# Kernel optimization log

Measured on AMD Instinct MI355X. Metric: run time of the kernel, lower is better.

The kernel has to match this reference:

```python
import jax, jax.numpy as jnp
import numpy as np

VOCAB_SIZE = 32000
PAD_IDX = 0


def setup_inputs() -> dict:
    key = jax.random.key(0)
    k1, k2 = jax.random.split(key)
    tokens = jax.random.randint(k1, (256, 2048), 0, VOCAB_SIZE, dtype=jnp.int64 if jax.config.jax_enable_x64 else jnp.int32)
    lengths = jax.random.randint(k2, (256,), 0, 2048, dtype=tokens.dtype)
    return {"tokens": tokens, "lengths": lengths}


def reference(tokens, lengths):
    # Faithful to torch OneHotEncoder.forward:
    #   onehot[b,t,:] = one_hot(tokens[b,t]) with pad_idx column zeroed per position,
    #   then summed over t -> counts [batch, vocab]. NOTE: the torch code computes a
    #   clamped `outhot` but RETURNS the un-clamped `onehot` counts; we match that.
    # Efficient form: direct per-row scatter-add histogram, skipping pad tokens,
    # without materializing the [B, T, V] intermediate.
    B, T = tokens.shape
    rows = jnp.arange(B)[:, None]  # [B,1] broadcasts against tokens [B,T]
    contrib = jnp.where(tokens == PAD_IDX, 0.0, 1.0).astype(jnp.float32)
    counts = jnp.zeros((B, VOCAB_SIZE), dtype=jnp.float32).at[rows, tokens].add(contrib)
    # pad_idx column is always zeroed (scatter of 0 at pad_selector per position)
    counts = counts.at[:, PAD_IDX].set(0.0)
    return counts
```

## Files before the change

### kernel.cpp

```cpp
#include <hip/hip_runtime.h>


#define VOCAB 32000
#define BLOCK 1024

__global__ __launch_bounds__(BLOCK)
void OneHotEncoder_43052752175267_kernel(const int* __restrict__ tokens,
                                         float* __restrict__ out,
                                         int T) {
    __shared__ __align__(16) unsigned int hist[VOCAB / 2];

    const int row = blockIdx.x;
    const int tid = threadIdx.x;

    uint4* h4 = (uint4*)hist;
    const uint4 z = make_uint4(0u, 0u, 0u, 0u);
    for (int i = tid; i < VOCAB / 8; i += BLOCK)
        h4[i] = z;
    __syncthreads();

    const int* trow = tokens + (long long)row * T;
    for (int i = tid; i < T; i += BLOCK) {
        int tok = trow[i];
        if (tok != 0)
            atomicAdd(&hist[tok >> 1], 1u << ((tok & 1) << 4));
    }
    __syncthreads();

    float4* o4 = (float4*)(out + (long long)row * VOCAB);
    const uint2* h2 = (const uint2*)hist;
    for (int i = tid; i < VOCAB / 4; i += BLOCK) {
        uint2 h = h2[i];
        float4 f;
        f.x = (float)(h.x & 0xFFFFu);
        f.y = (float)(h.x >> 16);
        f.z = (float)(h.y & 0xFFFFu);
        f.w = (float)(h.y >> 16);
        o4[i] = f;
    }
}

extern "C" void kernel_launch(void* const* d_in, const int* in_sizes, int n_in,
                              void* d_out, int out_size, void* d_ws, size_t ws_size,
                              hipStream_t stream) {
    const int* tokens = (const int*)d_in[0];
    const int B = in_sizes[1];
    const int T = in_sizes[0] / B;
    float* out = (float*)d_out;

    OneHotEncoder_43052752175267_kernel<<<dim3(B), dim3(BLOCK), 0, stream>>>(tokens, out, T);
}
```

Measured before the change: 65.71 us.

## Split vocab histogram into slices across blocks with vectorized token loads

Each row's histogram is split into 8 vocab slices, each handled by its own 256-thread block with a small shared histogram. Every block reads the whole token row as int4 and only counts tokens in its slice. This gives 8x more blocks and a much smaller LDS footprint, which raises occupancy and spreads the output writes across more blocks. The cost is that each token row is read 8 times, and the int4 path assumes T is divisible by 4.

```diff
diff --git a/kernel.cpp b/kernel.cpp
--- a/kernel.cpp
+++ b/kernel.cpp
@@ -2,34 +2,43 @@
 
 
 #define VOCAB 32000
-#define BLOCK 1024
+#define SLICES 8
+#define SLICE_BINS (VOCAB / SLICES)
+#define BLOCK 256
 
 __global__ __launch_bounds__(BLOCK)
 void OneHotEncoder_43052752175267_kernel(const int* __restrict__ tokens,
                                          float* __restrict__ out,
                                          int T) {
-    __shared__ __align__(16) unsigned int hist[VOCAB / 2];
+    __shared__ __align__(16) unsigned int hist[SLICE_BINS / 2];
 
-    const int row = blockIdx.x;
-    const int tid = threadIdx.x;
+    const int slice = blockIdx.x;
+    const int row   = blockIdx.y;
+    const int tid   = threadIdx.x;
+    const int base  = slice * SLICE_BINS;
 
     uint4* h4 = (uint4*)hist;
     const uint4 z = make_uint4(0u, 0u, 0u, 0u);
-    for (int i = tid; i < VOCAB / 8; i += BLOCK)
+    for (int i = tid; i < SLICE_BINS / 8; i += BLOCK)
         h4[i] = z;
     __syncthreads();
 
-    const int* trow = tokens + (long long)row * T;
-    for (int i = tid; i < T; i += BLOCK) {
-        int tok = trow[i];
-        if (tok != 0)
-            atomicAdd(&hist[tok >> 1], 1u << ((tok & 1) << 4));
+    const int4* trow4 = (const int4*)(tokens + (long long)row * T);
+    for (int i = tid; i < T / 4; i += BLOCK) {
+        int4 tk = trow4[i];
+        #pragma unroll
+        for (int j = 0; j < 4; ++j) {
+            int tok = (j == 0) ? tk.x : (j == 1) ? tk.y : (j == 2) ? tk.z : tk.w;
+            unsigned int local = (unsigned int)(tok - base);
+            if (local < SLICE_BINS && tok != 0)
+                atomicAdd(&hist[local >> 1], 1u << ((local & 1) << 4));
+        }
     }
     __syncthreads();
 
-    float4* o4 = (float4*)(out + (long long)row * VOCAB);
+    float4* o4 = (float4*)(out + (long long)row * VOCAB + base);
     const uint2* h2 = (const uint2*)hist;
-    for (int i = tid; i < VOCAB / 4; i += BLOCK) {
+    for (int i = tid; i < SLICE_BINS / 4; i += BLOCK) {
         uint2 h = h2[i];
         float4 f;
         f.x = (float)(h.x & 0xFFFFu);
@@ -48,5 +57,6 @@
     const int T = in_sizes[0] / B;
     float* out = (float*)d_out;
 
-    OneHotEncoder_43052752175267_kernel<<<dim3(B), dim3(BLOCK), 0, stream>>>(tokens, out, T);
+    OneHotEncoder_43052752175267_kernel<<<dim3(SLICES, B), dim3(BLOCK), 0, stream>>>(
+        tokens, out, T);
 }
```

Result: slower. 67.96 us (+3.4%).
